# Kernel tuning notes

Measured on AMD Instinct MI355X. Metric: run time of the kernel, lower is better.

## Reference

```python
import jax, jax.numpy as jnp
import numpy as np

WINDOW = 9
PAD = (WINDOW - 1) // 2


def setup_inputs() -> dict:
    key = jax.random.key(0)
    k1, k2 = jax.random.split(key)
    B, C, L, H = 32, 512, 4096, 8
    x = jax.random.normal(k1, (B, C, L), dtype=jnp.float32)
    W = jax.random.normal(k2, (H, C, WINDOW), dtype=jnp.float32) * (1.0 / np.sqrt(C * WINDOW))
    b = jnp.zeros((H,), dtype=jnp.float32)
    return {"x": x, "W": W, "b": b}


def reference(x, W, b):
    # conv1d: x [B,C,L], W [H,C,w] -> logits [B,H,L] (same padding, stride 1)
    logits = jax.lax.conv_general_dilated(
        x, W,
        window_strides=(1,),
        padding=[(PAD, PAD)],
        dimension_numbers=("NCH", "OIH", "NCH"),
    ) + b[None, :, None]
    # softmax over sequence length
    focus = jax.nn.softmax(logits, axis=-1)  # [B,H,L]
    # per-head weighted sum pooling over L: [B,C,H]
    pooled = jnp.einsum("bhl,bcl->bch", focus, x)
    # reduce='max' over heads -> [B,C]
    return jnp.max(pooled, axis=-1)
```

## Files before the change

### kernel.cpp

```cpp
#include <hip/hip_runtime.h>

#define B_LEN 32
#define C_LEN 512
#define L_LEN 4096
#define H_LEN 8
#define WIN 9

typedef __attribute__((ext_vector_type(8))) short short8v;
typedef __attribute__((ext_vector_type(4))) float float4v;

__device__ __forceinline__ short f2bf(float f) {
  unsigned u = __float_as_uint(f);
  unsigned r = (u + 0x7fffu + ((u >> 16) & 1u)) >> 16;
  return (short)r;
}

__global__ __launch_bounds__(256) void repack_w_bf16(
    const float* __restrict__ W, short* __restrict__ Wt)
{
  const int i = blockIdx.x * 256 + threadIdx.x;
  if (i >= WIN * 16 * C_LEN) return;
  const int c = i & 511;
  const int h = (i >> 9) & 15;
  const int w = i / (16 * C_LEN);
  const float v = (h < H_LEN) ? W[((size_t)h * C_LEN + c) * WIN + w] : 0.f;
  Wt[i] = f2bf(v);
}

#define SLICE 5760

__global__ __launch_bounds__(256, 3) void conv_mfma(
    const float* __restrict__ x, const short* __restrict__ Wt,
    float* __restrict__ part)
{
  __shared__ short xt[4 * 2 * (SLICE / 2)];
  const int t = threadIdx.x;
  const int lane = t & 63;
  const int wid = t >> 6;
  const int j15 = lane & 15;
  const int g = lane >> 4;
  const int g16 = g * 16;
  const int b = blockIdx.y;
  const int l0b = blockIdx.x * 256;
  const int wl0 = wid * 64;
  const int s = l0b + wl0 - 4;
  const float* xb = x + (size_t)b * C_LEN * L_LEN;

  char* bufA = (char*)&xt[0] + (size_t)wid * 2 * SLICE;
  char* bufB = bufA + SLICE;

  const int q = lane & 15;
  const int chigh = lane >> 4;
  const int bl = s + 4 + 4 * q;
  const int hside = lane >> 5;
  const int hc = lane & 31;
  const int hl = s + (hside ? 68 : 0);
  const bool hok = (hl >= 0) && (hl + 3 < L_LEN);
  const int hlc = hok ? hl : (hside ? (L_LEN - 4) : 0);
  const int hr = hside ? 68 : 0;
  const int hkey = hside ? 16 : 0;

  float4 L0, L1, L2, L3, L4, L5, L6, L7, LH;
  short8v wn0, wn1, wn2, wn3, wn4, wn5, wn6, wn7, wn8;
  const float4 z4 = make_float4(0.f, 0.f, 0.f, 0.f);

#define WLOAD(K)                                                               \
  {                                                                            \
    const short* Wb = Wt + (K) * 32 + j15 * 512 + 8 * g;                       \
    wn0 = *(const short8v*)(Wb);                                               \
    wn1 = *(const short8v*)(Wb + 1 * 8192);                                    \
    wn2 = *(const short8v*)(Wb + 2 * 8192);                                    \
    wn3 = *(const short8v*)(Wb + 3 * 8192);                                    \
    wn4 = *(const short8v*)(Wb + 4 * 8192);                                    \
    wn5 = *(const short8v*)(Wb + 5 * 8192);                                    \
    wn6 = *(const short8v*)(Wb + 6 * 8192);                                    \
    wn7 = *(const short8v*)(Wb + 7 * 8192);                                    \
    wn8 = *(const short8v*)(Wb + 8 * 8192);                                    \
  }

#define LOADK(K)                                                               \
  {                                                                            \
    const float* bsrc = xb + (size_t)((K) * 32 + chigh * 8) * L_LEN + bl;      \
    L0 = *(const float4*)(bsrc);                                               \
    L1 = *(const float4*)(bsrc + 1 * (size_t)L_LEN);                           \
    L2 = *(const float4*)(bsrc + 2 * (size_t)L_LEN);                           \
    L3 = *(const float4*)(bsrc + 3 * (size_t)L_LEN);                           \
    L4 = *(const float4*)(bsrc + 4 * (size_t)L_LEN);                           \
    L5 = *(const float4*)(bsrc + 5 * (size_t)L_LEN);                           \
    L6 = *(const float4*)(bsrc + 6 * (size_t)L_LEN);                           \
    L7 = *(const float4*)(bsrc + 7 * (size_t)L_LEN);                           \
    LH = *(const float4*)(xb + (size_t)((K) * 32 + hc) * L_LEN + hlc);         \
    if (!hok) LH = z4;                                                         \
  }

#define WROW(BB, E, CMP)                                                       \
  {                                                                            \
    const int r = 4 + 4 * q + (E);                                             \
    short8v v = { f2bf(L0.CMP), f2bf(L1.CMP), f2bf(L2.CMP), f2bf(L3.CMP),      \
                  f2bf(L4.CMP), f2bf(L5.CMP), f2bf(L6.CMP), f2bf(L7.CMP) };    \
    *(short8v*)((BB) + r * 80 + ((chigh * 16) ^ (((r >> 2) & 3) << 4))) = v;   \
  }

#define WRITEB(BB)                                                             \
  {                                                                            \
    WROW(BB, 0, x) WROW(BB, 1, y) WROW(BB, 2, z) WROW(BB, 3, w)                \
    *(short*)((BB) + (hr + 0) * 80 + ((hc * 2) ^ hkey)) = f2bf(LH.x);          \
    *(short*)((BB) + (hr + 1) * 80 + ((hc * 2) ^ hkey)) = f2bf(LH.y);          \
    *(short*)((BB) + (hr + 2) * 80 + ((hc * 2) ^ hkey)) = f2bf(LH.z);          \
    *(short*)((BB) + (hr + 3) * 80 + ((hc * 2) ^ hkey)) = f2bf(LH.w);          \
  }

#define MSTEP(BB, ROFF, ACC, WF)                                               \
  {                                                                            \
    const int r = rw + (ROFF);                                                 \
    short8v xf = *(const short8v*)((BB) + r * 80 + (g16 ^ (((r >> 2) & 3) << 4))); \
    ACC = __builtin_amdgcn_mfma_f32_16x16x32_bf16(WF, xf, ACC, 0, 0, 0);       \
  }

#define CSTEP(BB, W, WF)                                                       \
  {                                                                            \
    const int rw = j15 + (W);                                                  \
    MSTEP(BB, 0, acc0, WF) MSTEP(BB, 16, acc1, WF)                             \
    MSTEP(BB, 32, acc2, WF) MSTEP(BB, 48, acc3, WF)                            \
  }

#define COMPUTE(BB)                                                            \
  {                                                                            \
    CSTEP(BB, 0, wn0) CSTEP(BB, 1, wn1) CSTEP(BB, 2, wn2)                      \
    CSTEP(BB, 3, wn3) CSTEP(BB, 4, wn4) CSTEP(BB, 5, wn5)                      \
    CSTEP(BB, 6, wn6) CSTEP(BB, 7, wn7) CSTEP(BB, 8, wn8)                      \
  }

  float4v acc0 = {0.f, 0.f, 0.f, 0.f};
  float4v acc1 = acc0, acc2 = acc0, acc3 = acc0;

#define CK(I) (I)

  LOADK(CK(0))
  WRITEB(bufA)

  for (int i = 0; i < 16; i += 2) {
    WLOAD(CK(i))
    LOADK(CK(i + 1))
    COMPUTE(bufA)
    WRITEB(bufB)
    WLOAD(CK(i + 1))
    if (i + 2 < 16) { LOADK(CK(i + 2)) }
    COMPUTE(bufB)
    if (i + 2 < 16) { WRITEB(bufA) }
  }

  if (lane < 32) {
    float* d = part + ((size_t)b * H_LEN + 4 * g) * L_LEN + (l0b + wl0 + j15);
#pragma unroll
    for (int r = 0; r < 4; ++r) {
      d[(size_t)r * L_LEN +  0] = acc0[r];
      d[(size_t)r * L_LEN + 16] = acc1[r];
      d[(size_t)r * L_LEN + 32] = acc2[r];
      d[(size_t)r * L_LEN + 48] = acc3[r];
    }
  }
#undef WLOAD
#undef LOADK
#undef WROW
#undef WRITEB
#undef MSTEP
#undef CSTEP
#undef COMPUTE
#undef CK
}

__global__ __launch_bounds__(256) void softmax_rows(
    const float* __restrict__ part, float* __restrict__ focus)
{
  __shared__ float red[256];
  const int r = blockIdx.x;
  const int t = threadIdx.x;
  float v[16];
#pragma unroll
  for (int k = 0; k < 4; ++k) {
    const int i4 = (t + 256 * k) * 4;
    float4 a = *reinterpret_cast<const float4*>(&part[(size_t)r * L_LEN + i4]);
    v[4 * k + 0] = a.x; v[4 * k + 1] = a.y; v[4 * k + 2] = a.z; v[4 * k + 3] = a.w;
  }
  float m = v[0];
#pragma unroll
  for (int k = 1; k < 16; ++k) m = fmaxf(m, v[k]);
  red[t] = m;
  __syncthreads();
  for (int s = 128; s > 0; s >>= 1) {
    if (t < s) red[t] = fmaxf(red[t], red[t + s]);
    __syncthreads();
  }
  m = red[0];
  __syncthreads();
  float sum = 0.f;
#pragma unroll
  for (int k = 0; k < 16; ++k) { v[k] = __expf(v[k] - m); sum += v[k]; }
  red[t] = sum;
  __syncthreads();
  for (int s = 128; s > 0; s >>= 1) {
    if (t < s) red[t] += red[t + s];
    __syncthreads();
  }
  const float inv = 1.f / red[0];
#pragma unroll
  for (int k = 0; k < 4; ++k) {
    const int i4 = (t + 256 * k) * 4;
    float4 a;
    a.x = v[4 * k + 0] * inv; a.y = v[4 * k + 1] * inv;
    a.z = v[4 * k + 2] * inv; a.w = v[4 * k + 3] * inv;
    *reinterpret_cast<float4*>(&focus[(size_t)r * L_LEN + i4]) = a;
  }
}

#define K3_ST 68
#define K3_NS 4

__global__ __launch_bounds__(256) void pool_partial(
    const float* __restrict__ x, const float* __restrict__ focus,
    float* __restrict__ pool2)
{
  __shared__ float xs[64 * K3_ST];
  const int t = threadIdx.x;
  const int cl = t & 63;
  const int p = t >> 6;
  const int pu = __builtin_amdgcn_readfirstlane(p);
  const int b = blockIdx.y;
  const int c0 = blockIdx.x * 64;
  const int lbeg = blockIdx.z * (L_LEN / K3_NS);
  const float* f0 = focus + ((size_t)b * H_LEN + pu) * L_LEN;
  const float* f1 = f0 + 4 * (size_t)L_LEN;
  const float* xb = x + (size_t)b * C_LEN * L_LEN;
  const int srow = t >> 4;
  const int scol = (t & 15) * 4;
  float acc0 = 0.f, acc1 = 0.f;

  for (int l0 = lbeg; l0 < lbeg + L_LEN / K3_NS; l0 += 64) {
    __syncthreads();
#pragma unroll
    for (int pass = 0; pass < 4; ++pass) {
      const int c = srow + pass * 16;
      float4 v = *reinterpret_cast<const float4*>(&xb[(size_t)(c0 + c) * L_LEN + l0 + scol]);
      *reinterpret_cast<float4*>(&xs[c * K3_ST + scol]) = v;
    }
    __syncthreads();
#pragma unroll
    for (int l4 = 0; l4 < 16; ++l4) {
      const float4 xv = *reinterpret_cast<const float4*>(&xs[cl * K3_ST + 4 * l4]);
      const int li = l0 + 4 * l4;
      acc0 = fmaf(xv.x, f0[li + 0], acc0);
      acc0 = fmaf(xv.y, f0[li + 1], acc0);
      acc0 = fmaf(xv.z, f0[li + 2], acc0);
      acc0 = fmaf(xv.w, f0[li + 3], acc0);
      acc1 = fmaf(xv.x, f1[li + 0], acc1);
      acc1 = fmaf(xv.y, f1[li + 1], acc1);
      acc1 = fmaf(xv.z, f1[li + 2], acc1);
      acc1 = fmaf(xv.w, f1[li + 3], acc1);
    }
  }
  float* dst = pool2 + (((size_t)blockIdx.z * B_LEN + b) * C_LEN + c0 + cl) * H_LEN;
  dst[p] = acc0;
  dst[p + 4] = acc1;
}

__global__ __launch_bounds__(256) void pool_reduce(
    const float* __restrict__ pool2, float* __restrict__ out)
{
  const int i = blockIdx.x * 256 + threadIdx.x;
  float s[H_LEN];
#pragma unroll
  for (int h = 0; h < H_LEN; ++h) s[h] = 0.f;
  for (int ls = 0; ls < K3_NS; ++ls) {
    const float* src = pool2 + ((size_t)ls * B_LEN * C_LEN + i) * H_LEN;
    float4 a = *reinterpret_cast<const float4*>(src);
    float4 b4 = *reinterpret_cast<const float4*>(src + 4);
    s[0] += a.x; s[1] += a.y; s[2] += a.z; s[3] += a.w;
    s[4] += b4.x; s[5] += b4.y; s[6] += b4.z; s[7] += b4.w;
  }
  float m = s[0];
#pragma unroll
  for (int h = 1; h < H_LEN; ++h) m = fmaxf(m, s[h]);
  out[i] = m;
}

extern "C" void kernel_launch(void* const* d_in, const int* in_sizes, int n_in,
                              void* d_out, int out_size, void* d_ws, size_t ws_size,
                              hipStream_t stream)
{
  const float* x = (const float*)d_in[0];
  const float* W = (const float*)d_in[1];
  float* out = (float*)d_out;
  float* ws = (float*)d_ws;

  const size_t PART = (size_t)B_LEN * H_LEN * L_LEN;
  const size_t POOL2N = (size_t)K3_NS * B_LEN * C_LEN * H_LEN;

  float* part = ws;
  float* focus = ws + PART;
  float* pool2 = focus + PART;
  short* Wt = (short*)(pool2 + POOL2N);

  hipLaunchKernelGGL(repack_w_bf16, dim3((WIN * 16 * C_LEN + 255) / 256), dim3(256), 0,
                     stream, W, Wt);
  hipLaunchKernelGGL(conv_mfma, dim3(L_LEN / 256, B_LEN), dim3(256), 0,
                     stream, x, Wt, part);
  hipLaunchKernelGGL(softmax_rows, dim3(B_LEN * H_LEN), dim3(256), 0,
                     stream, part, focus);
  hipLaunchKernelGGL(pool_partial, dim3(C_LEN / 64, B_LEN, K3_NS), dim3(256), 0,
                     stream, x, focus, pool2);
  hipLaunchKernelGGL(pool_reduce, dim3((B_LEN * C_LEN) / 256), dim3(256), 0,
                     stream, pool2, out);
}
```

Before: 135.2 us.

## Double-buffer conv register prefetch two chunks ahead, lower occupancy to two

```diff
diff --git a/kernel.cpp b/kernel.cpp
--- a/kernel.cpp
+++ b/kernel.cpp
@@ -29,7 +29,7 @@
 
 #define SLICE 5760
 
-__global__ __launch_bounds__(256, 3) void conv_mfma(
+__global__ __launch_bounds__(256, 2) void conv_mfma(
     const float* __restrict__ x, const short* __restrict__ Wt,
     float* __restrict__ part)
 {
@@ -60,54 +60,58 @@
   const int hr = hside ? 68 : 0;
   const int hkey = hside ? 16 : 0;
 
-  float4 L0, L1, L2, L3, L4, L5, L6, L7, LH;
-  short8v wn0, wn1, wn2, wn3, wn4, wn5, wn6, wn7, wn8;
+  float4 xA0, xA1, xA2, xA3, xA4, xA5, xA6, xA7, xAH;
+  float4 xB0, xB1, xB2, xB3, xB4, xB5, xB6, xB7, xBH;
+  short8v wA0, wA1, wA2, wA3, wA4, wA5, wA6, wA7, wA8;
+  short8v wB0, wB1, wB2, wB3, wB4, wB5, wB6, wB7, wB8;
   const float4 z4 = make_float4(0.f, 0.f, 0.f, 0.f);
 
-#define WLOAD(K)                                                               \
+#define WLOAD(S, K)                                                            \
   {                                                                            \
     const short* Wb = Wt + (K) * 32 + j15 * 512 + 8 * g;                       \
-    wn0 = *(const short8v*)(Wb);                                               \
-    wn1 = *(const short8v*)(Wb + 1 * 8192);                                    \
-    wn2 = *(const short8v*)(Wb + 2 * 8192);                                    \
-    wn3 = *(const short8v*)(Wb + 3 * 8192);                                    \
-    wn4 = *(const short8v*)(Wb + 4 * 8192);                                    \
-    wn5 = *(const short8v*)(Wb + 5 * 8192);                                    \
-    wn6 = *(const short8v*)(Wb + 6 * 8192);                                    \
-    wn7 = *(const short8v*)(Wb + 7 * 8192);                                    \
-    wn8 = *(const short8v*)(Wb + 8 * 8192);                                    \
-  }
-
-#define LOADK(K)                                                               \
+    (w##S##0) = *(const short8v*)(Wb);                                         \
+    (w##S##1) = *(const short8v*)(Wb + 1 * 8192);                              \
+    (w##S##2) = *(const short8v*)(Wb + 2 * 8192);                              \
+    (w##S##3) = *(const short8v*)(Wb + 3 * 8192);                              \
+    (w##S##4) = *(const short8v*)(Wb + 4 * 8192);                              \
+    (w##S##5) = *(const short8v*)(Wb + 5 * 8192);                              \
+    (w##S##6) = *(const short8v*)(Wb + 6 * 8192);                              \
+    (w##S##7) = *(const short8v*)(Wb + 7 * 8192);                              \
+    (w##S##8) = *(const short8v*)(Wb + 8 * 8192);                              \
+  }
+
+#define LOADK(S, K)                                                            \
   {                                                                            \
     const float* bsrc = xb + (size_t)((K) * 32 + chigh * 8) * L_LEN + bl;      \
-    L0 = *(const float4*)(bsrc);                                               \
-    L1 = *(const float4*)(bsrc + 1 * (size_t)L_LEN);                           \
-    L2 = *(const float4*)(bsrc + 2 * (size_t)L_LEN);                           \
-    L3 = *(const float4*)(bsrc + 3 * (size_t)L_LEN);                           \
-    L4 = *(const float4*)(bsrc + 4 * (size_t)L_LEN);                           \
-    L5 = *(const float4*)(bsrc + 5 * (size_t)L_LEN);                           \
-    L6 = *(const float4*)(bsrc + 6 * (size_t)L_LEN);                           \
-    L7 = *(const float4*)(bsrc + 7 * (size_t)L_LEN);                           \
-    LH = *(const float4*)(xb + (size_t)((K) * 32 + hc) * L_LEN + hlc);         \
-    if (!hok) LH = z4;                                                         \
-  }
-
-#define WROW(BB, E, CMP)                                                       \
+    (x##S##0) = *(const float4*)(bsrc);                                        \
+    (x##S##1) = *(const float4*)(bsrc + 1 * (size_t)L_LEN);                    \
+    (x##S##2) = *(const float4*)(bsrc + 2 * (size_t)L_LEN);                    \
+    (x##S##3) = *(const float4*)(bsrc + 3 * (size_t)L_LEN);                    \
+    (x##S##4) = *(const float4*)(bsrc + 4 * (size_t)L_LEN);                    \
+    (x##S##5) = *(const float4*)(bsrc + 5 * (size_t)L_LEN);                    \
+    (x##S##6) = *(const float4*)(bsrc + 6 * (size_t)L_LEN);                    \
+    (x##S##7) = *(const float4*)(bsrc + 7 * (size_t)L_LEN);                    \
+    (x##S##H) = *(const float4*)(xb + (size_t)((K) * 32 + hc) * L_LEN + hlc);  \
+    if (!hok) (x##S##H) = z4;                                                  \
+  }
+
+#define WROW(S, BB, E, CMP)                                                    \
   {                                                                            \
     const int r = 4 + 4 * q + (E);                                             \
-    short8v v = { f2bf(L0.CMP), f2bf(L1.CMP), f2bf(L2.CMP), f2bf(L3.CMP),      \
-                  f2bf(L4.CMP), f2bf(L5.CMP), f2bf(L6.CMP), f2bf(L7.CMP) };    \
+    short8v v = { f2bf((x##S##0).CMP), f2bf((x##S##1).CMP),                    \
+                  f2bf((x##S##2).CMP), f2bf((x##S##3).CMP),                    \
+                  f2bf((x##S##4).CMP), f2bf((x##S##5).CMP),                    \
+                  f2bf((x##S##6).CMP), f2bf((x##S##7).CMP) };                  \
     *(short8v*)((BB) + r * 80 + ((chigh * 16) ^ (((r >> 2) & 3) << 4))) = v;   \
   }
 
-#define WRITEB(BB)                                                             \
-  {                                                                            \
-    WROW(BB, 0, x) WROW(BB, 1, y) WROW(BB, 2, z) WROW(BB, 3, w)                \
-    *(short*)((BB) + (hr + 0) * 80 + ((hc * 2) ^ hkey)) = f2bf(LH.x);          \
-    *(short*)((BB) + (hr + 1) * 80 + ((hc * 2) ^ hkey)) = f2bf(LH.y);          \
-    *(short*)((BB) + (hr + 2) * 80 + ((hc * 2) ^ hkey)) = f2bf(LH.z);          \
-    *(short*)((BB) + (hr + 3) * 80 + ((hc * 2) ^ hkey)) = f2bf(LH.w);          \
+#define WRITEB(S, BB)                                                          \
+  {                                                                            \
+    WROW(S, BB, 0, x) WROW(S, BB, 1, y) WROW(S, BB, 2, z) WROW(S, BB, 3, w)    \
+    *(short*)((BB) + (hr + 0) * 80 + ((hc * 2) ^ hkey)) = f2bf((x##S##H).x);   \
+    *(short*)((BB) + (hr + 1) * 80 + ((hc * 2) ^ hkey)) = f2bf((x##S##H).y);   \
+    *(short*)((BB) + (hr + 2) * 80 + ((hc * 2) ^ hkey)) = f2bf((x##S##H).z);   \
+    *(short*)((BB) + (hr + 3) * 80 + ((hc * 2) ^ hkey)) = f2bf((x##S##H).w);   \
   }
 
 #define MSTEP(BB, ROFF, ACC, WF)                                               \
@@ -124,30 +128,30 @@
     MSTEP(BB, 32, acc2, WF) MSTEP(BB, 48, acc3, WF)                            \
   }
 
-#define COMPUTE(BB)                                                            \
-  {                                                                            \
-    CSTEP(BB, 0, wn0) CSTEP(BB, 1, wn1) CSTEP(BB, 2, wn2)                      \
-    CSTEP(BB, 3, wn3) CSTEP(BB, 4, wn4) CSTEP(BB, 5, wn5)                      \
-    CSTEP(BB, 6, wn6) CSTEP(BB, 7, wn7) CSTEP(BB, 8, wn8)                      \
+#define COMPUTE(BB, S)                                                         \
+  {                                                                            \
+    CSTEP(BB, 0, (w##S##0)) CSTEP(BB, 1, (w##S##1)) CSTEP(BB, 2, (w##S##2))    \
+    CSTEP(BB, 3, (w##S##3)) CSTEP(BB, 4, (w##S##4)) CSTEP(BB, 5, (w##S##5))    \
+    CSTEP(BB, 6, (w##S##6)) CSTEP(BB, 7, (w##S##7)) CSTEP(BB, 8, (w##S##8))    \
   }
 
   float4v acc0 = {0.f, 0.f, 0.f, 0.f};
   float4v acc1 = acc0, acc2 = acc0, acc3 = acc0;
 
-#define CK(I) (I)
-
-  LOADK(CK(0))
-  WRITEB(bufA)
+  LOADK(A, 0)
+  WLOAD(A, 0)
+  LOADK(B, 1)
+  WRITEB(A, bufA)
 
   for (int i = 0; i < 16; i += 2) {
-    WLOAD(CK(i))
-    LOADK(CK(i + 1))
-    COMPUTE(bufA)
-    WRITEB(bufB)
-    WLOAD(CK(i + 1))
-    if (i + 2 < 16) { LOADK(CK(i + 2)) }
-    COMPUTE(bufB)
-    if (i + 2 < 16) { WRITEB(bufA) }
+    WLOAD(B, i + 1)
+    if (i + 2 < 16) { LOADK(A, i + 2) }
+    COMPUTE(bufA, A)
+    WRITEB(B, bufB)
+    if (i + 2 < 16) { WLOAD(A, i + 2) }
+    if (i + 3 < 16) { LOADK(B, i + 3) }
+    COMPUTE(bufB, B)
+    if (i + 2 < 16) { WRITEB(A, bufA) }
   }
 
   if (lane < 32) {
@@ -167,7 +171,6 @@
 #undef MSTEP
 #undef CSTEP
 #undef COMPUTE
-#undef CK
 }
 
 __global__ __launch_bounds__(256) void softmax_rows(
@@ -236,7 +239,7 @@
   const int scol = (t & 15) * 4;
   float acc0 = 0.f, acc1 = 0.f;
 
-  for (int l0 = lbeg; l0 < lbeg + L_LEN / K3_NS; l0 += 64) {
+  for (int l0 = 0 + blockIdx.z * (L_LEN / K3_NS); l0 < lbeg + L_LEN / K3_NS; l0 += 64) {
     __syncthreads();
 #pragma unroll
     for (int pass = 0; pass < 4; ++pass) {
```

New measurement: 142.7 us. 1.06x slower.
